# Kernel tuning notes

Measured on AMD Instinct MI355X. Metric: run time of the kernel, lower is better.

## Reference

```python
import jax, jax.numpy as jnp
import numpy as np

N_NODES = 50000
N_EDGES = 800000
D_IN = 64
D_HID = 64
D_OUT = 64


def setup_inputs() -> dict:
    key = jax.random.key(0)
    ks = jax.random.split(key, 6)
    X = jax.random.normal(ks[0], (N_NODES, D_IN), dtype=jnp.float32)
    edge_index = jax.random.randint(ks[1], (2, N_EDGES), 0, N_NODES, dtype=jnp.int64)
    edge_weight = jax.random.uniform(ks[2], (N_EDGES,), dtype=jnp.float32)
    W1 = jax.random.normal(ks[3], (D_IN, D_HID), dtype=jnp.float32) / np.float32(np.sqrt(D_IN))
    b1 = jnp.zeros((D_HID,), dtype=jnp.float32)
    W2 = jax.random.normal(ks[4], (D_HID, D_OUT), dtype=jnp.float32) / np.float32(np.sqrt(D_HID))
    b2 = jnp.zeros((D_OUT,), dtype=jnp.float32)
    return {"X": X, "edge_weight": edge_weight, "W1": W1, "b1": b1,
            "W2": W2, "b2": b2, "edge_index": edge_index}


def reference(X, edge_weight, W1, b1, W2, b2, edge_index):
    # conv(A, X) = (A @ X) @ W + b with sparse A given as (edge_index, edge_weight)
    src = edge_index[0]
    dst = edge_index[1]

    def agg(H):
        # weighted neighborhood sum: [E, d] messages scattered to [N, d]
        msgs = edge_weight[:, None] * H[src]
        return jax.ops.segment_sum(msgs, dst, num_segments=N_NODES)

    # layer 1: conv -> relu (dropout p=0 is identity)
    H = jax.nn.relu(agg(X) @ W1 + b1)
    # last layer: conv, no final activation (l_act=None)
    return agg(H) @ W2 + b2
```

## Files before the change

kernel.cpp:

```cpp
#include <hip/hip_runtime.h>

#define D 64

template <bool PRE>
__global__ __launch_bounds__(256, 4) void gemm64_kernel(
    const float* __restrict__ A, const float* __restrict__ W,
    const float* __restrict__ bpre, float* __restrict__ out, int N) {
  __shared__ float sA[64][68];
  __shared__ float sW[64][68];
  const int t = threadIdx.x;
  const int rowBase = blockIdx.x * 64;

#pragma unroll
  for (int i = t * 4; i < 4096; i += 1024) {
    const int k = i >> 6, c = i & 63;
    *reinterpret_cast<float4*>(&sW[k][c]) =
        *reinterpret_cast<const float4*>(W + i);
  }
#pragma unroll
  for (int i = t * 4; i < 4096; i += 1024) {
    const int r = i >> 6, k = i & 63;
    const int row = rowBase + r;
    float4 a = make_float4(0.f, 0.f, 0.f, 0.f);
    if (row < N) a = *reinterpret_cast<const float4*>(A + (size_t)row * D + k);
    if (PRE) {
      const float4 b = *reinterpret_cast<const float4*>(bpre + k);
      a.x = fmaxf(a.x + b.x, 0.f);
      a.y = fmaxf(a.y + b.y, 0.f);
      a.z = fmaxf(a.z + b.z, 0.f);
      a.w = fmaxf(a.w + b.w, 0.f);
    }
    *reinterpret_cast<float4*>(&sA[r][k]) = a;
  }
  __syncthreads();

  const int ty = t >> 4, tx = t & 15;
  float4 acc0 = make_float4(0.f, 0.f, 0.f, 0.f);
  float4 acc1 = make_float4(0.f, 0.f, 0.f, 0.f);
  float4 acc2 = make_float4(0.f, 0.f, 0.f, 0.f);
  float4 acc3 = make_float4(0.f, 0.f, 0.f, 0.f);

#pragma unroll 4
  for (int kq = 0; kq < 16; ++kq) {
    const float4 w0 = *reinterpret_cast<const float4*>(&sW[kq * 4 + 0][tx * 4]);
    const float4 w1 = *reinterpret_cast<const float4*>(&sW[kq * 4 + 1][tx * 4]);
    const float4 w2 = *reinterpret_cast<const float4*>(&sW[kq * 4 + 2][tx * 4]);
    const float4 w3 = *reinterpret_cast<const float4*>(&sW[kq * 4 + 3][tx * 4]);
    const float4 a0 = *reinterpret_cast<const float4*>(&sA[ty * 4 + 0][kq * 4]);
    const float4 a1 = *reinterpret_cast<const float4*>(&sA[ty * 4 + 1][kq * 4]);
    const float4 a2 = *reinterpret_cast<const float4*>(&sA[ty * 4 + 2][kq * 4]);
    const float4 a3 = *reinterpret_cast<const float4*>(&sA[ty * 4 + 3][kq * 4]);
#define FMA4(ACC, AV)                                                     \
    ACC.x += AV.x * w0.x + AV.y * w1.x + AV.z * w2.x + AV.w * w3.x;       \
    ACC.y += AV.x * w0.y + AV.y * w1.y + AV.z * w2.y + AV.w * w3.y;       \
    ACC.z += AV.x * w0.z + AV.y * w1.z + AV.z * w2.z + AV.w * w3.z;       \
    ACC.w += AV.x * w0.w + AV.y * w1.w + AV.z * w2.w + AV.w * w3.w;
    FMA4(acc0, a0) FMA4(acc1, a1) FMA4(acc2, a2) FMA4(acc3, a3)
#undef FMA4
  }

  const int row0 = rowBase + ty * 4;
  if (row0 + 0 < N) *reinterpret_cast<float4*>(out + (size_t)(row0 + 0) * D + tx * 4) = acc0;
  if (row0 + 1 < N) *reinterpret_cast<float4*>(out + (size_t)(row0 + 1) * D + tx * 4) = acc1;
  if (row0 + 2 < N) *reinterpret_cast<float4*>(out + (size_t)(row0 + 2) * D + tx * 4) = acc2;
  if (row0 + 3 < N) *reinterpret_cast<float4*>(out + (size_t)(row0 + 3) * D + tx * 4) = acc3;
}

__global__ __launch_bounds__(256, 4) void agg_gemm_kernel(
    const float* __restrict__ H, const int* __restrict__ offs,
    const int2* __restrict__ pairs, const float* __restrict__ b1,
    const float* __restrict__ W, float* __restrict__ out, int N) {
  __shared__ float sA[64][68];
  __shared__ float sW[64][68];
  const int t = threadIdx.x;
  const int rowBase = blockIdx.x * 64;

#pragma unroll
  for (int i = t * 4; i < 4096; i += 1024) {
    const int k = i >> 6, c = i & 63;
    *reinterpret_cast<float4*>(&sW[k][c]) =
        *reinterpret_cast<const float4*>(W + i);
  }

  const int l4 = t & 15;
  const int sub = t >> 4;
  const float4 bb = *reinterpret_cast<const float4*>(b1 + l4 * 4);
#pragma unroll
  for (int p = 0; p < 4; ++p) {
    const int r = p * 16 + sub;
    const int node = rowBase + r;
    float4 A0 = make_float4(0.f, 0.f, 0.f, 0.f);
    float4 A1 = make_float4(0.f, 0.f, 0.f, 0.f);
    float4 A2 = make_float4(0.f, 0.f, 0.f, 0.f);
    float4 A3 = make_float4(0.f, 0.f, 0.f, 0.f);
    if (node < N) {
      const int beg = offs[node], end = offs[node + 1];
      int i = beg;
      for (; i + 4 <= end; i += 4) {
        const int2 p0 = pairs[i], p1 = pairs[i + 1], p2 = pairs[i + 2], p3 = pairs[i + 3];
        const float4 v0 = *reinterpret_cast<const float4*>(H + (size_t)p0.x * D + l4 * 4);
        const float4 v1 = *reinterpret_cast<const float4*>(H + (size_t)p1.x * D + l4 * 4);
        const float4 v2 = *reinterpret_cast<const float4*>(H + (size_t)p2.x * D + l4 * 4);
        const float4 v3 = *reinterpret_cast<const float4*>(H + (size_t)p3.x * D + l4 * 4);
        const float w0 = __int_as_float(p0.y), w1 = __int_as_float(p1.y);
        const float w2 = __int_as_float(p2.y), w3 = __int_as_float(p3.y);
        A0.x += w0 * v0.x; A0.y += w0 * v0.y; A0.z += w0 * v0.z; A0.w += w0 * v0.w;
        A1.x += w1 * v1.x; A1.y += w1 * v1.y; A1.z += w1 * v1.z; A1.w += w1 * v1.w;
        A2.x += w2 * v2.x; A2.y += w2 * v2.y; A2.z += w2 * v2.z; A2.w += w2 * v2.w;
        A3.x += w3 * v3.x; A3.y += w3 * v3.y; A3.z += w3 * v3.z; A3.w += w3 * v3.w;
      }
      for (; i < end; ++i) {
        const int2 pp = pairs[i];
        const float4 v = *reinterpret_cast<const float4*>(H + (size_t)pp.x * D + l4 * 4);
        const float w = __int_as_float(pp.y);
        A0.x += w * v.x; A0.y += w * v.y; A0.z += w * v.z; A0.w += w * v.w;
      }
    }
    float4 rr;
    rr.x = fmaxf((A0.x + A1.x) + (A2.x + A3.x) + bb.x, 0.f);
    rr.y = fmaxf((A0.y + A1.y) + (A2.y + A3.y) + bb.y, 0.f);
    rr.z = fmaxf((A0.z + A1.z) + (A2.z + A3.z) + bb.z, 0.f);
    rr.w = fmaxf((A0.w + A1.w) + (A2.w + A3.w) + bb.w, 0.f);
    *reinterpret_cast<float4*>(&sA[r][l4 * 4]) = rr;
  }
  __syncthreads();

  const int ty = t >> 4, tx = t & 15;
  float4 acc0 = make_float4(0.f, 0.f, 0.f, 0.f);
  float4 acc1 = make_float4(0.f, 0.f, 0.f, 0.f);
  float4 acc2 = make_float4(0.f, 0.f, 0.f, 0.f);
  float4 acc3 = make_float4(0.f, 0.f, 0.f, 0.f);

#pragma unroll 4
  for (int kq = 0; kq < 16; ++kq) {
    const float4 w0 = *reinterpret_cast<const float4*>(&sW[kq * 4 + 0][tx * 4]);
    const float4 w1 = *reinterpret_cast<const float4*>(&sW[kq * 4 + 1][tx * 4]);
    const float4 w2 = *reinterpret_cast<const float4*>(&sW[kq * 4 + 2][tx * 4]);
    const float4 w3 = *reinterpret_cast<const float4*>(&sW[kq * 4 + 3][tx * 4]);
    const float4 a0 = *reinterpret_cast<const float4*>(&sA[ty * 4 + 0][kq * 4]);
    const float4 a1 = *reinterpret_cast<const float4*>(&sA[ty * 4 + 1][kq * 4]);
    const float4 a2 = *reinterpret_cast<const float4*>(&sA[ty * 4 + 2][kq * 4]);
    const float4 a3 = *reinterpret_cast<const float4*>(&sA[ty * 4 + 3][kq * 4]);
#define FMA4(ACC, AV)                                                     \
    ACC.x += AV.x * w0.x + AV.y * w1.x + AV.z * w2.x + AV.w * w3.x;       \
    ACC.y += AV.x * w0.y + AV.y * w1.y + AV.z * w2.y + AV.w * w3.y;       \
    ACC.z += AV.x * w0.z + AV.y * w1.z + AV.z * w2.z + AV.w * w3.z;       \
    ACC.w += AV.x * w0.w + AV.y * w1.w + AV.z * w2.w + AV.w * w3.w;
    FMA4(acc0, a0) FMA4(acc1, a1) FMA4(acc2, a2) FMA4(acc3, a3)
#undef FMA4
  }

  const int row0 = rowBase + ty * 4;
  if (row0 + 0 < N) *reinterpret_cast<float4*>(out + (size_t)(row0 + 0) * D + tx * 4) = acc0;
  if (row0 + 1 < N) *reinterpret_cast<float4*>(out + (size_t)(row0 + 1) * D + tx * 4) = acc1;
  if (row0 + 2 < N) *reinterpret_cast<float4*>(out + (size_t)(row0 + 2) * D + tx * 4) = acc2;
  if (row0 + 3 < N) *reinterpret_cast<float4*>(out + (size_t)(row0 + 3) * D + tx * 4) = acc3;
}

__global__ __launch_bounds__(256) void hist_kernel(
    const int* __restrict__ dst, int* __restrict__ deg,
    int* __restrict__ posw, int E) {
  int e = blockIdx.x * 256 + threadIdx.x;
  if (e < E) posw[e] = atomicAdd(&deg[dst[e]], 1);
}

#define SCAN_CHUNK 1024
__global__ __launch_bounds__(256) void scan_part_kernel(
    const int* __restrict__ deg, int* __restrict__ offs,
    int* __restrict__ bsums, int N) {
  __shared__ int s[256];
  const int t = threadIdx.x;
  const int base = blockIdx.x * SCAN_CHUNK + t * 4;
  int v0 = 0, v1 = 0, v2 = 0, v3 = 0;
  if (base + 3 < N) {
    const int4 v = *reinterpret_cast<const int4*>(deg + base);
    v0 = v.x; v1 = v.y; v2 = v.z; v3 = v.w;
  } else {
    if (base + 0 < N) v0 = deg[base + 0];
    if (base + 1 < N) v1 = deg[base + 1];
    if (base + 2 < N) v2 = deg[base + 2];
  }
  const int tsum = v0 + v1 + v2 + v3;
  s[t] = tsum;
  __syncthreads();
  for (int off = 1; off < 256; off <<= 1) {
    int x = (t >= off) ? s[t - off] : 0;
    __syncthreads();
    s[t] += x;
    __syncthreads();
  }
  const int excl = s[t] - tsum;
  if (base + 0 < N) offs[base + 0] = excl;
  if (base + 1 < N) offs[base + 1] = excl + v0;
  if (base + 2 < N) offs[base + 2] = excl + v0 + v1;
  if (base + 3 < N) offs[base + 3] = excl + v0 + v1 + v2;
  if (t == 255) bsums[blockIdx.x] = s[255];
}

__global__ __launch_bounds__(1024) void scan_sums_kernel(
    int* __restrict__ bsums, int* __restrict__ offsN, int nb) {
  __shared__ int s[1024];
  const int t = threadIdx.x;
  const int v = (t < nb) ? bsums[t] : 0;
  s[t] = v;
  __syncthreads();
  for (int off = 1; off < 1024; off <<= 1) {
    int x = (t >= off) ? s[t - off] : 0;
    __syncthreads();
    s[t] += x;
    __syncthreads();
  }
  if (t < nb) bsums[t] = s[t] - v;
  if (t == nb - 1) *offsN = s[t];
}

__global__ __launch_bounds__(256) void scan_add_kernel(
    int* __restrict__ offs, const int* __restrict__ bsums, int N) {
  const int i = blockIdx.x * 256 + threadIdx.x;
  if (i < N) offs[i] += bsums[i >> 10];
}

__global__ __launch_bounds__(256) void bucket_kernel(
    const int* __restrict__ src, const int* __restrict__ dst,
    const float* __restrict__ ew, const int* __restrict__ offs,
    const int* __restrict__ posw, int2* __restrict__ pairs, int E) {
  int e = blockIdx.x * 256 + threadIdx.x;
  if (e < E) {
    const int pos = offs[dst[e]] + posw[e];
    pairs[pos] = make_int2(src[e], __float_as_int(ew[e]));
  }
}

#define NB 256
#define RB 256

__global__ __launch_bounds__(256) void p1_hist_kernel(
    const int* __restrict__ dst, int* __restrict__ countsT, int E, int epb) {
  __shared__ int h[RB];
  const int t = threadIdx.x;
  h[t] = 0;
  __syncthreads();
  const int base = blockIdx.x * epb;
  const int lim = min(base + epb, E);
  for (int i = base + t; i < lim; i += 256) atomicAdd(&h[dst[i] >> 8], 1);
  __syncthreads();
  countsT[t * NB + blockIdx.x] = h[t];
}

__global__ __launch_bounds__(256) void p1_scatter_kernel(
    const int* __restrict__ src, const int* __restrict__ dst,
    const float* __restrict__ ew, const int* __restrict__ SC,
    const int* __restrict__ bsums, int2* __restrict__ tmp, int E, int epb) {
  __shared__ int cur[RB];
  const int t = threadIdx.x;
  const int idx = t * NB + blockIdx.x;
  cur[t] = SC[idx] + bsums[idx >> 10];
  __syncthreads();
  const int base = blockIdx.x * epb;
  const int lim = min(base + epb, E);
  for (int i = base + t; i < lim; i += 256) {
    const int d = dst[i];
    const unsigned s = (unsigned)src[i];
    const float w = ew[i];
    const int pos = atomicAdd(&cur[d >> 8], 1);
    tmp[pos] = make_int2((int)((unsigned)d | (s << 16)), __float_as_int(w));
  }
}

__global__ __launch_bounds__(256) void p2_kernel(
    const int2* __restrict__ tmp, const int* __restrict__ SC,
    const int* __restrict__ bsums,
    int* __restrict__ offs, int2* __restrict__ pairs, int N, int E) {
  __shared__ int h[RB];
  __shared__ int s[RB];
  __shared__ int cur[RB];
  const int t = threadIdx.x;
  const int b = blockIdx.x;
  const int segBeg = SC[b * RB] + bsums[b >> 2];
  const int segEnd = (b == RB - 1) ? E : (SC[(b + 1) * RB] + bsums[(b + 1) >> 2]);

  h[t] = 0;
  __syncthreads();
  for (int i = segBeg + t; i < segEnd; i += 256)
    atomicAdd(&h[tmp[i].x & 255], 1);
  __syncthreads();

  const int v = h[t];
  s[t] = v;
  __syncthreads();
  for (int off = 1; off < 256; off <<= 1) {
    int x = (t >= off) ? s[t - off] : 0;
    __syncthreads();
    s[t] += x;
    __syncthreads();
  }
  const int excl = s[t] - v;
  cur[t] = segBeg + excl;
  const int node = b * RB + t;
  if (node <= N) offs[node] = segBeg + excl;
  __syncthreads();

  for (int i = segBeg + t; i < segEnd; i += 256) {
    const int2 r = tmp[i];
    const int lo = r.x & 255;
    const int pos = atomicAdd(&cur[lo], 1);
    pairs[pos] = make_int2((int)(((unsigned)r.x) >> 16), r.y);
  }
}

template <bool BIAS>
__global__ __launch_bounds__(256) void gather_agg_kernel(
    const float* __restrict__ H, const int* __restrict__ offs,
    const int2* __restrict__ pairs,
    const float* __restrict__ bias, float* __restrict__ out, int N) {
  const int l4 = threadIdx.x & 15;
  const int node = blockIdx.x * 16 + (threadIdx.x >> 4);
  if (node >= N) return;
  const int beg = offs[node], end = offs[node + 1];
  float4 A0 = make_float4(0.f, 0.f, 0.f, 0.f);
  float4 A1 = make_float4(0.f, 0.f, 0.f, 0.f);
  float4 A2 = make_float4(0.f, 0.f, 0.f, 0.f);
  float4 A3 = make_float4(0.f, 0.f, 0.f, 0.f);
  int i = beg;
  for (; i + 4 <= end; i += 4) {
    const int2 p0 = pairs[i], p1 = pairs[i + 1], p2 = pairs[i + 2], p3 = pairs[i + 3];
    const float4 v0 = *reinterpret_cast<const float4*>(H + (size_t)p0.x * D + l4 * 4);
    const float4 v1 = *reinterpret_cast<const float4*>(H + (size_t)p1.x * D + l4 * 4);
    const float4 v2 = *reinterpret_cast<const float4*>(H + (size_t)p2.x * D + l4 * 4);
    const float4 v3 = *reinterpret_cast<const float4*>(H + (size_t)p3.x * D + l4 * 4);
    const float w0 = __int_as_float(p0.y), w1 = __int_as_float(p1.y);
    const float w2 = __int_as_float(p2.y), w3 = __int_as_float(p3.y);
    A0.x += w0 * v0.x; A0.y += w0 * v0.y; A0.z += w0 * v0.z; A0.w += w0 * v0.w;
    A1.x += w1 * v1.x; A1.y += w1 * v1.y; A1.z += w1 * v1.z; A1.w += w1 * v1.w;
    A2.x += w2 * v2.x; A2.y += w2 * v2.y; A2.z += w2 * v2.z; A2.w += w2 * v2.w;
    A3.x += w3 * v3.x; A3.y += w3 * v3.y; A3.z += w3 * v3.z; A3.w += w3 * v3.w;
  }
  for (; i < end; ++i) {
    const int2 p = pairs[i];
    const float4 v = *reinterpret_cast<const float4*>(H + (size_t)p.x * D + l4 * 4);
    const float w = __int_as_float(p.y);
    A0.x += w * v.x; A0.y += w * v.y; A0.z += w * v.z; A0.w += w * v.w;
  }
  float4 r;
  r.x = (A0.x + A1.x) + (A2.x + A3.x);
  r.y = (A0.y + A1.y) + (A2.y + A3.y);
  r.z = (A0.z + A1.z) + (A2.z + A3.z);
  r.w = (A0.w + A1.w) + (A2.w + A3.w);
  if (BIAS) {
    const float4 b = *reinterpret_cast<const float4*>(bias + l4 * 4);
    r.x += b.x; r.y += b.y; r.z += b.z; r.w += b.w;
  }
  *reinterpret_cast<float4*>(out + (size_t)node * D + l4 * 4) = r;
}

__global__ __launch_bounds__(256) void scatter_kernel(
    const float* __restrict__ H, const float* __restrict__ ew,
    const int* __restrict__ src, const int* __restrict__ dst,
    float* __restrict__ out, int nEdges) {
  const int tid = blockIdx.x * 256 + threadIdx.x;
  const int e = tid >> 4;
  if (e >= nEdges) return;
  const int c = (tid & 15) * 4;
  const float w = ew[e];
  const float4 v = *reinterpret_cast<const float4*>(H + (size_t)src[e] * D + c);
  float* o = out + (size_t)dst[e] * D + c;
  atomicAdd(o + 0, w * v.x);
  atomicAdd(o + 1, w * v.y);
  atomicAdd(o + 2, w * v.z);
  atomicAdd(o + 3, w * v.w);
}

__global__ __launch_bounds__(256) void fill_bias_kernel(
    float* __restrict__ out, const float* __restrict__ b, int total) {
  int i = blockIdx.x * 256 + threadIdx.x;
  if (i < total) out[i] = b[i & 63];
}

extern "C" void kernel_launch(void* const* d_in, const int* in_sizes, int n_in,
                              void* d_out, int out_size, void* d_ws,
                              size_t ws_size, hipStream_t stream) {
  const float* X  = (const float*)d_in[0];
  const float* ew = (const float*)d_in[1];
  const float* W1 = (const float*)d_in[2];
  const float* b1 = (const float*)d_in[3];
  const float* W2 = (const float*)d_in[4];
  const float* b2 = (const float*)d_in[5];
  const int*   ei = (const int*)d_in[6];

  const int N = in_sizes[0] / D;
  const int E = in_sizes[6] / 2;
  const int* src = ei;
  const int* dst = ei + E;
  float* out = (float*)d_out;

  char* ws = (char*)d_ws;
  float* buf0 = (float*)ws;                 ws += (size_t)N * D * 4;
  float* buf1 = (float*)ws;                 ws += (size_t)N * D * 4;
  const size_t baseBytes = (size_t)(ws - (char*)d_ws);
  int2*  pairs  = (int2*)ws;                ws += (size_t)E * 8;
  int*   offs   = (int*)ws;                 ws += (size_t)(N + 1) * 4;
  const size_t needBytes = (size_t)(ws - (char*)d_ws);

  const int gemmBlocks = (N + 63) / 64;
  const int aggBlocks  = (N + 15) / 16;
  const int edgeBlocks = (E + 255) / 256;

  if (ws_size >= needBytes) {
    if (N <= 65536 && (size_t)N * D * 4 >= (size_t)(2 * NB * RB + 1 + 64) * 4 &&
        (size_t)N * D * 4 >= (size_t)E * 8) {
      int*  countsT = (int*)buf0;
      int*  SC      = (int*)buf0 + NB * RB;
      int*  bsums   = (int*)buf0 + 2 * NB * RB + 1;
      int2* tmp     = (int2*)buf1;

      const int epb = (E + NB - 1) / NB;
      p1_hist_kernel<<<NB, 256, 0, stream>>>(dst, countsT, E, epb);
      scan_part_kernel<<<NB * RB / SCAN_CHUNK, 256, 0, stream>>>(countsT, SC, bsums, NB * RB);
      scan_sums_kernel<<<1, 1024, 0, stream>>>(bsums, SC + NB * RB, NB * RB / SCAN_CHUNK);
      p1_scatter_kernel<<<NB, 256, 0, stream>>>(src, dst, ew, SC, bsums, tmp, E, epb);
      p2_kernel<<<RB, 256, 0, stream>>>(tmp, SC, bsums, offs, pairs, N, E);
    } else {
      int* deg   = (int*)buf0;
      int* bsums = (int*)buf0 + N;
      int* posw  = (int*)buf1;
      const int nb = (N + SCAN_CHUNK - 1) / SCAN_CHUNK;
      hipMemsetAsync(deg, 0, (size_t)N * 4, stream);
      hist_kernel<<<edgeBlocks, 256, 0, stream>>>(dst, deg, posw, E);
      scan_part_kernel<<<nb, 256, 0, stream>>>(deg, offs, bsums, N);
      scan_sums_kernel<<<1, 1024, 0, stream>>>(bsums, offs + N, nb);
      scan_add_kernel<<<(N + 255) / 256, 256, 0, stream>>>(offs, bsums, N);
      bucket_kernel<<<edgeBlocks, 256, 0, stream>>>(src, dst, ew, offs, posw, pairs, E);
    }

    gemm64_kernel<false><<<gemmBlocks, 256, 0, stream>>>(X, W1, nullptr, buf0, N);
    agg_gemm_kernel<<<gemmBlocks, 256, 0, stream>>>(buf0, offs, pairs, b1, W2, buf1, N);
    gather_agg_kernel<true><<<aggBlocks, 256, 0, stream>>>(buf1, offs, pairs, b2, out, N);
  } else if (ws_size >= baseBytes) {
    const int scatBlocks = (E * 16 + 255) / 256;
    const int fillBlocks = (N * D + 255) / 256;
    gemm64_kernel<false><<<gemmBlocks, 256, 0, stream>>>(X, W1, nullptr, buf0, N);
    hipMemsetAsync(buf1, 0, (size_t)N * D * 4, stream);
    scatter_kernel<<<scatBlocks, 256, 0, stream>>>(buf0, ew, src, dst, buf1, E);
    gemm64_kernel<true><<<gemmBlocks, 256, 0, stream>>>(buf1, W2, b1, buf0, N);
    fill_bias_kernel<<<fillBlocks, 256, 0, stream>>>(out, b2, N * D);
    scatter_kernel<<<scatBlocks, 256, 0, stream>>>(buf0, ew, src, dst, out, E);
  }
}
```

Measured before the change: 117.2 us.

## Fuse bucket histogram with first GEMM and fold scan into scatter kernel

The coarse-bin histogram now shares a launch with the X@W1 GEMM: the first NB blocks count edges per bin and the rest compute the GEMM. The separate two-kernel prefix scan is dropped, and each p1_scatter block instead sums the NB per-block counts for its bin and runs a 256-wide scan itself. This removes three kernel launches and their dependency gaps. In exchange every scatter block repeats the 256x256 count read and scan, and countsB/binBaseG need extra workspace, so the sort path and its ws_size check change.

```diff
diff --git a/kernel.cpp b/kernel.cpp
--- a/kernel.cpp
+++ b/kernel.cpp
@@ -1,6 +1,9 @@
 #include <hip/hip_runtime.h>
 
 #define D 64
+
+#define NB 256
+#define RB 256
 
 template <bool PRE>
 __global__ __launch_bounds__(256, 4) void gemm64_kernel(
@@ -64,6 +67,232 @@
   if (row0 + 1 < N) *reinterpret_cast<float4*>(out + (size_t)(row0 + 1) * D + tx * 4) = acc1;
   if (row0 + 2 < N) *reinterpret_cast<float4*>(out + (size_t)(row0 + 2) * D + tx * 4) = acc2;
   if (row0 + 3 < N) *reinterpret_cast<float4*>(out + (size_t)(row0 + 3) * D + tx * 4) = acc3;
+}
+
+__global__ __launch_bounds__(256, 4) void hist_gemm_kernel(
+    const int* __restrict__ dst, int* __restrict__ countsB, int E, int epb,
+    const float* __restrict__ A, const float* __restrict__ W,
+    float* __restrict__ out, int N) {
+  __shared__ float sA[64][68];
+  __shared__ float sW[64][68];
+  const int t = threadIdx.x;
+
+  if ((int)blockIdx.x < NB) {
+    int* h = reinterpret_cast<int*>(&sA[0][0]);
+    h[t] = 0;
+    __syncthreads();
+    const int base = blockIdx.x * epb;
+    const int lim = min(base + epb, E);
+    for (int i = base + t; i < lim; i += 256) atomicAdd(&h[dst[i] >> 8], 1);
+    __syncthreads();
+    countsB[blockIdx.x * RB + t] = h[t];
+    return;
+  }
+
+  const int rowBase = ((int)blockIdx.x - NB) * 64;
+#pragma unroll
+  for (int i = t * 4; i < 4096; i += 1024) {
+    const int k = i >> 6, c = i & 63;
+    *reinterpret_cast<float4*>(&sW[k][c]) =
+        *reinterpret_cast<const float4*>(W + i);
+  }
+#pragma unroll
+  for (int i = t * 4; i < 4096; i += 1024) {
+    const int r = i >> 6, k = i & 63;
+    const int row = rowBase + r;
+    float4 a = make_float4(0.f, 0.f, 0.f, 0.f);
+    if (row < N) a = *reinterpret_cast<const float4*>(A + (size_t)row * D + k);
+    *reinterpret_cast<float4*>(&sA[r][k]) = a;
+  }
+  __syncthreads();
+
+  const int ty = t >> 4, tx = t & 15;
+  float4 acc0 = make_float4(0.f, 0.f, 0.f, 0.f);
+  float4 acc1 = make_float4(0.f, 0.f, 0.f, 0.f);
+  float4 acc2 = make_float4(0.f, 0.f, 0.f, 0.f);
+  float4 acc3 = make_float4(0.f, 0.f, 0.f, 0.f);
+
+#pragma unroll 4
+  for (int kq = 0; kq < 16; ++kq) {
+    const float4 w0 = *reinterpret_cast<const float4*>(&sW[kq * 4 + 0][tx * 4]);
+    const float4 w1 = *reinterpret_cast<const float4*>(&sW[kq * 4 + 1][tx * 4]);
+    const float4 w2 = *reinterpret_cast<const float4*>(&sW[kq * 4 + 2][tx * 4]);
+    const float4 w3 = *reinterpret_cast<const float4*>(&sW[kq * 4 + 3][tx * 4]);
+    const float4 a0 = *reinterpret_cast<const float4*>(&sA[ty * 4 + 0][kq * 4]);
+    const float4 a1 = *reinterpret_cast<const float4*>(&sA[ty * 4 + 1][kq * 4]);
+    const float4 a2 = *reinterpret_cast<const float4*>(&sA[ty * 4 + 2][kq * 4]);
+    const float4 a3 = *reinterpret_cast<const float4*>(&sA[ty * 4 + 3][kq * 4]);
+#define FMA4(ACC, AV)                                                     \
+    ACC.x += AV.x * w0.x + AV.y * w1.x + AV.z * w2.x + AV.w * w3.x;       \
+    ACC.y += AV.x * w0.y + AV.y * w1.y + AV.z * w2.y + AV.w * w3.y;       \
+    ACC.z += AV.x * w0.z + AV.y * w1.z + AV.z * w2.z + AV.w * w3.z;       \
+    ACC.w += AV.x * w0.w + AV.y * w1.w + AV.z * w2.w + AV.w * w3.w;
+    FMA4(acc0, a0) FMA4(acc1, a1) FMA4(acc2, a2) FMA4(acc3, a3)
+#undef FMA4
+  }
+
+  const int row0 = rowBase + ty * 4;
+  if (row0 + 0 < N) *reinterpret_cast<float4*>(out + (size_t)(row0 + 0) * D + tx * 4) = acc0;
+  if (row0 + 1 < N) *reinterpret_cast<float4*>(out + (size_t)(row0 + 1) * D + tx * 4) = acc1;
+  if (row0 + 2 < N) *reinterpret_cast<float4*>(out + (size_t)(row0 + 2) * D + tx * 4) = acc2;
+  if (row0 + 3 < N) *reinterpret_cast<float4*>(out + (size_t)(row0 + 3) * D + tx * 4) = acc3;
+}
+
+__global__ __launch_bounds__(256) void p1_scatter_kernel(
+    const int* __restrict__ src, const int* __restrict__ dst,
+    const float* __restrict__ ew, const int* __restrict__ countsB,
+    int* __restrict__ binBaseG, int2* __restrict__ tmp, int E, int epb) {
+  __shared__ int s[RB];
+  __shared__ int cur[RB];
+  const int t = threadIdx.x;
+  const int b = blockIdx.x;
+
+  int total = 0, pre = 0;
+#pragma unroll 8
+  for (int i = 0; i < NB; ++i) {
+    const int c = countsB[i * RB + t];
+    if (i == b) pre = total;
+    total += c;
+  }
+  s[t] = total;
+  __syncthreads();
+  for (int off = 1; off < 256; off <<= 1) {
+    int x = (t >= off) ? s[t - off] : 0;
+    __syncthreads();
+    s[t] += x;
+    __syncthreads();
+  }
+  const int binBase = s[t] - total;
+  cur[t] = binBase + pre;
+  if (b == 0) {
+    binBaseG[t] = binBase;
+    if (t == 255) binBaseG[256] = s[255];
+  }
+  __syncthreads();
+
+  const int base = b * epb;
+  const int lim = min(base + epb, E);
+  for (int i = base + t; i < lim; i += 256) {
+    const int d = dst[i];
+    const unsigned sv = (unsigned)src[i];
+    const float w = ew[i];
+    const int pos = atomicAdd(&cur[d >> 8], 1);
+    tmp[pos] = make_int2((int)((unsigned)d | (sv << 16)), __float_as_int(w));
+  }
+}
+
+__global__ __launch_bounds__(256) void p2_kernel(
+    const int2* __restrict__ tmp, const int* __restrict__ binBaseG,
+    int* __restrict__ offs, int2* __restrict__ pairs, int N) {
+  __shared__ int h[RB];
+  __shared__ int s[RB];
+  __shared__ int cur[RB];
+  const int t = threadIdx.x;
+  const int b = blockIdx.x;
+  const int segBeg = binBaseG[b];
+  const int segEnd = binBaseG[b + 1];
+
+  h[t] = 0;
+  __syncthreads();
+  for (int i = segBeg + t; i < segEnd; i += 256)
+    atomicAdd(&h[tmp[i].x & 255], 1);
+  __syncthreads();
+
+  const int v = h[t];
+  s[t] = v;
+  __syncthreads();
+  for (int off = 1; off < 256; off <<= 1) {
+    int x = (t >= off) ? s[t - off] : 0;
+    __syncthreads();
+    s[t] += x;
+    __syncthreads();
+  }
+  const int excl = s[t] - v;
+  cur[t] = segBeg + excl;
+  const int node = b * RB + t;
+  if (node <= N) offs[node] = segBeg + excl;
+  __syncthreads();
+
+  for (int i = segBeg + t; i < segEnd; i += 256) {
+    const int2 r = tmp[i];
+    const int lo = r.x & 255;
+    const int pos = atomicAdd(&cur[lo], 1);
+    pairs[pos] = make_int2((int)(((unsigned)r.x) >> 16), r.y);
+  }
+}
+
+__global__ __launch_bounds__(256) void hist_kernel(
+    const int* __restrict__ dst, int* __restrict__ deg,
+    int* __restrict__ posw, int E) {
+  int e = blockIdx.x * 256 + threadIdx.x;
+  if (e < E) posw[e] = atomicAdd(&deg[dst[e]], 1);
+}
+
+#define SCAN_CHUNK 1024
+__global__ __launch_bounds__(256) void scan_part_kernel(
+    const int* __restrict__ deg, int* __restrict__ offs,
+    int* __restrict__ bsums, int N) {
+  __shared__ int s[256];
+  const int t = threadIdx.x;
+  const int base = blockIdx.x * SCAN_CHUNK + t * 4;
+  int v0 = 0, v1 = 0, v2 = 0, v3 = 0;
+  if (base + 3 < N) {
+    const int4 v = *reinterpret_cast<const int4*>(deg + base);
+    v0 = v.x; v1 = v.y; v2 = v.z; v3 = v.w;
+  } else {
+    if (base + 0 < N) v0 = deg[base + 0];
+    if (base + 1 < N) v1 = deg[base + 1];
+    if (base + 2 < N) v2 = deg[base + 2];
+  }
+  const int tsum = v0 + v1 + v2 + v3;
+  s[t] = tsum;
+  __syncthreads();
+  for (int off = 1; off < 256; off <<= 1) {
+    int x = (t >= off) ? s[t - off] : 0;
+    __syncthreads();
+    s[t] += x;
+    __syncthreads();
+  }
+  const int excl = s[t] - tsum;
+  if (base + 0 < N) offs[base + 0] = excl;
+  if (base + 1 < N) offs[base + 1] = excl + v0;
+  if (base + 2 < N) offs[base + 2] = excl + v0 + v1;
+  if (base + 3 < N) offs[base + 3] = excl + v0 + v1 + v2;
+  if (t == 255) bsums[blockIdx.x] = s[255];
+}
+
+__global__ __launch_bounds__(1024) void scan_sums_kernel(
+    int* __restrict__ bsums, int* __restrict__ offsN, int nb) {
+  __shared__ int s[1024];
+  const int t = threadIdx.x;
+  const int v = (t < nb) ? bsums[t] : 0;
+  s[t] = v;
+  __syncthreads();
+  for (int off = 1; off < 1024; off <<= 1) {
+    int x = (t >= off) ? s[t - off] : 0;
+    __syncthreads();
+    s[t] += x;
+    __syncthreads();
+  }
+  if (t < nb) bsums[t] = s[t] - v;
+  if (t == nb - 1) *offsN = s[t];
+}
+
+__global__ __launch_bounds__(256) void scan_add_kernel(
+    int* __restrict__ offs, const int* __restrict__ bsums, int N) {
+  const int i = blockIdx.x * 256 + threadIdx.x;
+  if (i < N) offs[i] += bsums[i >> 10];
+}
+
+__global__ __launch_bounds__(256) void bucket_kernel(
+    const int* __restrict__ src, const int* __restrict__ dst,
+    const float* __restrict__ ew, const int* __restrict__ offs,
+    const int* __restrict__ posw, int2* __restrict__ pairs, int E) {
+  int e = blockIdx.x * 256 + threadIdx.x;
+  if (e < E) {
+    const int pos = offs[dst[e]] + posw[e];
+    pairs[pos] = make_int2(src[e], __float_as_int(ew[e]));
+  }
 }
 
 __global__ __launch_bounds__(256, 4) void agg_gemm_kernel(
@@ -157,157 +386,6 @@
   if (row0 + 3 < N) *reinterpret_cast<float4*>(out + (size_t)(row0 + 3) * D + tx * 4) = acc3;
 }
 
-__global__ __launch_bounds__(256) void hist_kernel(
-    const int* __restrict__ dst, int* __restrict__ deg,
-    int* __restrict__ posw, int E) {
-  int e = blockIdx.x * 256 + threadIdx.x;
-  if (e < E) posw[e] = atomicAdd(&deg[dst[e]], 1);
-}
-
-#define SCAN_CHUNK 1024
-__global__ __launch_bounds__(256) void scan_part_kernel(
-    const int* __restrict__ deg, int* __restrict__ offs,
-    int* __restrict__ bsums, int N) {
-  __shared__ int s[256];
-  const int t = threadIdx.x;
-  const int base = blockIdx.x * SCAN_CHUNK + t * 4;
-  int v0 = 0, v1 = 0, v2 = 0, v3 = 0;
-  if (base + 3 < N) {
-    const int4 v = *reinterpret_cast<const int4*>(deg + base);
-    v0 = v.x; v1 = v.y; v2 = v.z; v3 = v.w;
-  } else {
-    if (base + 0 < N) v0 = deg[base + 0];
-    if (base + 1 < N) v1 = deg[base + 1];
-    if (base + 2 < N) v2 = deg[base + 2];
-  }
-  const int tsum = v0 + v1 + v2 + v3;
-  s[t] = tsum;
-  __syncthreads();
-  for (int off = 1; off < 256; off <<= 1) {
-    int x = (t >= off) ? s[t - off] : 0;
-    __syncthreads();
-    s[t] += x;
-    __syncthreads();
-  }
-  const int excl = s[t] - tsum;
-  if (base + 0 < N) offs[base + 0] = excl;
-  if (base + 1 < N) offs[base + 1] = excl + v0;
-  if (base + 2 < N) offs[base + 2] = excl + v0 + v1;
-  if (base + 3 < N) offs[base + 3] = excl + v0 + v1 + v2;
-  if (t == 255) bsums[blockIdx.x] = s[255];
-}
-
-__global__ __launch_bounds__(1024) void scan_sums_kernel(
-    int* __restrict__ bsums, int* __restrict__ offsN, int nb) {
-  __shared__ int s[1024];
-  const int t = threadIdx.x;
-  const int v = (t < nb) ? bsums[t] : 0;
-  s[t] = v;
-  __syncthreads();
-  for (int off = 1; off < 1024; off <<= 1) {
-    int x = (t >= off) ? s[t - off] : 0;
-    __syncthreads();
-    s[t] += x;
-    __syncthreads();
-  }
-  if (t < nb) bsums[t] = s[t] - v;
-  if (t == nb - 1) *offsN = s[t];
-}
-
-__global__ __launch_bounds__(256) void scan_add_kernel(
-    int* __restrict__ offs, const int* __restrict__ bsums, int N) {
-  const int i = blockIdx.x * 256 + threadIdx.x;
-  if (i < N) offs[i] += bsums[i >> 10];
-}
-
-__global__ __launch_bounds__(256) void bucket_kernel(
-    const int* __restrict__ src, const int* __restrict__ dst,
-    const float* __restrict__ ew, const int* __restrict__ offs,
-    const int* __restrict__ posw, int2* __restrict__ pairs, int E) {
-  int e = blockIdx.x * 256 + threadIdx.x;
-  if (e < E) {
-    const int pos = offs[dst[e]] + posw[e];
-    pairs[pos] = make_int2(src[e], __float_as_int(ew[e]));
-  }
-}
-
-#define NB 256
-#define RB 256
-
-__global__ __launch_bounds__(256) void p1_hist_kernel(
-    const int* __restrict__ dst, int* __restrict__ countsT, int E, int epb) {
-  __shared__ int h[RB];
-  const int t = threadIdx.x;
-  h[t] = 0;
-  __syncthreads();
-  const int base = blockIdx.x * epb;
-  const int lim = min(base + epb, E);
-  for (int i = base + t; i < lim; i += 256) atomicAdd(&h[dst[i] >> 8], 1);
-  __syncthreads();
-  countsT[t * NB + blockIdx.x] = h[t];
-}
-
-__global__ __launch_bounds__(256) void p1_scatter_kernel(
-    const int* __restrict__ src, const int* __restrict__ dst,
-    const float* __restrict__ ew, const int* __restrict__ SC,
-    const int* __restrict__ bsums, int2* __restrict__ tmp, int E, int epb) {
-  __shared__ int cur[RB];
-  const int t = threadIdx.x;
-  const int idx = t * NB + blockIdx.x;
-  cur[t] = SC[idx] + bsums[idx >> 10];
-  __syncthreads();
-  const int base = blockIdx.x * epb;
-  const int lim = min(base + epb, E);
-  for (int i = base + t; i < lim; i += 256) {
-    const int d = dst[i];
-    const unsigned s = (unsigned)src[i];
-    const float w = ew[i];
-    const int pos = atomicAdd(&cur[d >> 8], 1);
-    tmp[pos] = make_int2((int)((unsigned)d | (s << 16)), __float_as_int(w));
-  }
-}
-
-__global__ __launch_bounds__(256) void p2_kernel(
-    const int2* __restrict__ tmp, const int* __restrict__ SC,
-    const int* __restrict__ bsums,
-    int* __restrict__ offs, int2* __restrict__ pairs, int N, int E) {
-  __shared__ int h[RB];
-  __shared__ int s[RB];
-  __shared__ int cur[RB];
-  const int t = threadIdx.x;
-  const int b = blockIdx.x;
-  const int segBeg = SC[b * RB] + bsums[b >> 2];
-  const int segEnd = (b == RB - 1) ? E : (SC[(b + 1) * RB] + bsums[(b + 1) >> 2]);
-
-  h[t] = 0;
-  __syncthreads();
-  for (int i = segBeg + t; i < segEnd; i += 256)
-    atomicAdd(&h[tmp[i].x & 255], 1);
-  __syncthreads();
-
-  const int v = h[t];
-  s[t] = v;
-  __syncthreads();
-  for (int off = 1; off < 256; off <<= 1) {
-    int x = (t >= off) ? s[t - off] : 0;
-    __syncthreads();
-    s[t] += x;
-    __syncthreads();
-  }
-  const int excl = s[t] - v;
-  cur[t] = segBeg + excl;
-  const int node = b * RB + t;
-  if (node <= N) offs[node] = segBeg + excl;
-  __syncthreads();
-
-  for (int i = segBeg + t; i < segEnd; i += 256) {
-    const int2 r = tmp[i];
-    const int lo = r.x & 255;
-    const int pos = atomicAdd(&cur[lo], 1);
-    pairs[pos] = make_int2((int)(((unsigned)r.x) >> 16), r.y);
-  }
-}
-
 template <bool BIAS>
 __global__ __launch_bounds__(256) void gather_agg_kernel(
     const float* __restrict__ H, const int* __restrict__ offs,
@@ -397,8 +475,10 @@
   float* buf0 = (float*)ws;                 ws += (size_t)N * D * 4;
   float* buf1 = (float*)ws;                 ws += (size_t)N * D * 4;
   const size_t baseBytes = (size_t)(ws - (char*)d_ws);
-  int2*  pairs  = (int2*)ws;                ws += (size_t)E * 8;
-  int*   offs   = (int*)ws;                 ws += (size_t)(N + 1) * 4;
+  int2*  pairs    = (int2*)ws;              ws += (size_t)E * 8;
+  int*   offs     = (int*)ws;               ws += (size_t)(N + 1) * 4;
+  int*   countsB  = (int*)ws;               ws += (size_t)NB * RB * 4;
+  int*   binBaseG = (int*)ws;               ws += (size_t)(RB + 1) * 4;
   const size_t needBytes = (size_t)(ws - (char*)d_ws);
 
   const int gemmBlocks = (N + 63) / 64;
@@ -406,19 +486,14 @@
   const int edgeBlocks = (E + 255) / 256;
 
   if (ws_size >= needBytes) {
-    if (N <= 65536 && (size_t)N * D * 4 >= (size_t)(2 * NB * RB + 1 + 64) * 4 &&
-        (size_t)N * D * 4 >= (size_t)E * 8) {
-      int*  countsT = (int*)buf0;
-      int*  SC      = (int*)buf0 + NB * RB;
-      int*  bsums   = (int*)buf0 + 2 * NB * RB + 1;
-      int2* tmp     = (int2*)buf1;
-
+    if (N <= NB * RB && (size_t)N * D * 4 >= (size_t)E * 8) {
+      int2* tmp = (int2*)buf1;
       const int epb = (E + NB - 1) / NB;
-      p1_hist_kernel<<<NB, 256, 0, stream>>>(dst, countsT, E, epb);
-      scan_part_kernel<<<NB * RB / SCAN_CHUNK, 256, 0, stream>>>(countsT, SC, bsums, NB * RB);
-      scan_sums_kernel<<<1, 1024, 0, stream>>>(bsums, SC + NB * RB, NB * RB / SCAN_CHUNK);
-      p1_scatter_kernel<<<NB, 256, 0, stream>>>(src, dst, ew, SC, bsums, tmp, E, epb);
-      p2_kernel<<<RB, 256, 0, stream>>>(tmp, SC, bsums, offs, pairs, N, E);
+      hist_gemm_kernel<<<NB + gemmBlocks, 256, 0, stream>>>(
+          dst, countsB, E, epb, X, W1, buf0, N);
+      p1_scatter_kernel<<<NB, 256, 0, stream>>>(src, dst, ew, countsB,
+                                                binBaseG, tmp, E, epb);
+      p2_kernel<<<RB, 256, 0, stream>>>(tmp, binBaseG, offs, pairs, N);
     } else {
       int* deg   = (int*)buf0;
       int* bsums = (int*)buf0 + N;
@@ -430,9 +505,9 @@
       scan_sums_kernel<<<1, 1024, 0, stream>>>(bsums, offs + N, nb);
       scan_add_kernel<<<(N + 255) / 256, 256, 0, stream>>>(offs, bsums, N);
       bucket_kernel<<<edgeBlocks, 256, 0, stream>>>(src, dst, ew, offs, posw, pairs, E);
+      gemm64_kernel<false><<<gemmBlocks, 256, 0, stream>>>(X, W1, nullptr, buf0, N);
     }
 
-    gemm64_kernel<false><<<gemmBlocks, 256, 0, stream>>>(X, W1, nullptr, buf0, N);
     agg_gemm_kernel<<<gemmBlocks, 256, 0, stream>>>(buf0, offs, pairs, b1, W2, buf1, N);
     gather_agg_kernel<true><<<aggBlocks, 256, 0, stream>>>(buf1, offs, pairs, b2, out, N);
   } else if (ws_size >= baseBytes) {
```

New measurement: 116.3 us. About the same (-0.7%).
